# Kernel optimization log

Hardware: AMD Instinct MI355X
Metric: run time of the kernel (lower is better)

Reference implementation:

```python
import jax, jax.numpy as jnp
import numpy as np

B, S, D = 4, 2048, 1024
H, DK = 16, 64           # n_heads, d_kv; inner_dim = H*DK = 1024 = D
R = 16
SCALING = 32.0 / R       # lora_alpha / r = 2.0


def setup_inputs() -> dict:
    key = jax.random.key(0)
    ks = jax.random.split(key, 10)
    inner = H * DK
    sd = 1.0 / np.sqrt(D)
    return {
        "hidden_states": jax.random.normal(ks[0], (B, S, D), jnp.float32),
        "position_bias": jax.random.normal(ks[1], (1, H, S, S), jnp.float32),
        "Wq": jax.random.normal(ks[2], (inner, D), jnp.float32) * sd,
        "Wk": jax.random.normal(ks[3], (inner, D), jnp.float32) * sd,
        "Wv": jax.random.normal(ks[4], (inner, D), jnp.float32) * sd,
        "Wo": jax.random.normal(ks[5], (D, inner), jnp.float32) * sd,
        "Aq": jax.random.normal(ks[6], (R, D), jnp.float32) * sd,
        "Bq": jax.random.normal(ks[7], (inner, R), jnp.float32) * 0.01,
        "Av": jax.random.normal(ks[8], (R, D), jnp.float32) * sd,
        "Bv": jax.random.normal(ks[9], (inner, R), jnp.float32) * 0.01,
    }


def reference(hidden_states, position_bias, Wq, Wk, Wv, Wo, Aq, Bq, Av, Bv):
    x = hidden_states  # [B,S,D]

    def lora(w_a, w_b):
        # ((x @ A^T) @ B^T) * scaling; low-rank path, rank R
        return ((x @ w_a.T) @ w_b.T) * SCALING

    def heads(t):  # [B,S,H*DK] -> [B,H,S,DK]
        return t.reshape(B, S, H, DK).transpose(0, 2, 1, 3)

    q = heads(x @ Wq.T + lora(Aq, Bq))
    k = heads(x @ Wk.T)
    v = heads(x @ Wv.T + lora(Av, Bv))

    # T5-style: no 1/sqrt(d) scaling; additive position bias
    scores = jnp.einsum("bhqd,bhkd->bhqk", q, k) + position_bias
    attn = jax.nn.softmax(scores, axis=-1)
    out = jnp.einsum("bhqk,bhkd->bhqd", attn, v)
    out = out.transpose(0, 2, 1, 3).reshape(B, S, H * DK)
    return out @ Wo.T
```

## Files before the change

### kernel.cpp

```cpp
#include <hip/hip_runtime.h>
#include <hip/hip_bf16.h>

typedef __bf16 bf16x8 __attribute__((ext_vector_type(8)));
typedef float  f32x4  __attribute__((ext_vector_type(4)));
typedef unsigned short u16;
typedef unsigned long long u64;

#define L2E 1.44269504089f

__device__ __forceinline__ u16 f2b(float f) {
    __bf16 h = (__bf16)f;
    return __builtin_bit_cast(u16, h);
}

typedef const __attribute__((address_space(1))) void* gas1_t;
typedef __attribute__((address_space(3))) void* las3_t;

__device__ __forceinline__ void gl_lds16(const void* g, void* l) {
    __builtin_amdgcn_global_load_lds((gas1_t)g, (las3_t)l, 16, 0, 0);
}


__global__ void cvt_bf16(const float* __restrict__ in, u16* __restrict__ out, int n4) {
    int i = blockIdx.x * 256 + threadIdx.x;
    if (i < n4) {
        float4 v = ((const float4*)in)[i];
        u64 pk = (u64)f2b(v.x) | ((u64)f2b(v.y) << 16) | ((u64)f2b(v.z) << 32) | ((u64)f2b(v.w) << 48);
        ((u64*)out)[i] = pk;
    }
}

__global__ void prep_wqkv(const float* __restrict__ Wq, const float* __restrict__ Wk,
                          const float* __restrict__ Wv, const float* __restrict__ Aq,
                          const float* __restrict__ Bq, const float* __restrict__ Av,
                          const float* __restrict__ Bv, u16* __restrict__ out) {
    int idx = blockIdx.x * 256 + threadIdx.x;
    int n = idx >> 10, j = idx & 1023;
    float v;
    if (n < 1024) {
        v = Wq[n * 1024 + j];
        const float* Br = Bq + n * 16;
        float s = 0.f;
#pragma unroll
        for (int r = 0; r < 16; ++r) s += Br[r] * Aq[r * 1024 + j];
        v += 2.0f * s;
    } else if (n < 2048) {
        v = Wk[(n - 1024) * 1024 + j];
    } else {
        int nn = n - 2048;
        v = Wv[nn * 1024 + j];
        const float* Br = Bv + nn * 16;
        float s = 0.f;
#pragma unroll
        for (int r = 0; r < 16; ++r) s += Br[r] * Av[r * 1024 + j];
        v += 2.0f * s;
    }
    out[idx] = f2b(v);
}


template <int EPI>
__global__ __launch_bounds__(256, 2)
void gemm_bt(const u16* __restrict__ A, const u16* __restrict__ W,
             float* __restrict__ Cout,
             u16* __restrict__ qo, u16* __restrict__ ko, u16* __restrict__ vo,
             int M, int N, int K) {
    __shared__ u16 ldsA[128 * 32];
    __shared__ u16 ldsW[128 * 32];
    const int t = threadIdx.x;
    const int l = t & 63;
    const int m0 = blockIdx.y * 128;
    const int n0 = blockIdx.x * 128;
    const int wm = (t >> 6) >> 1, wn = (t >> 6) & 1;
    const int lc = l & 15, lg = l >> 4;

    const int srow = t >> 2;
    const int sby = ((t & 3) * 16) ^ ((srow & 3) << 4);
    const size_t Ar0 = (size_t)(m0 + srow) * K, Ar1 = (size_t)(m0 + srow + 64) * K;
    const size_t Wr0 = (size_t)(n0 + srow) * K, Wr1 = (size_t)(n0 + srow + 64) * K;
    char* dA = (char*)ldsA;
    char* dW = (char*)ldsW;
    const int d0 = srow * 64 + (t & 3) * 16;
    const int d1 = d0 + 4096;

    f32x4 acc[4][4];
#pragma unroll
    for (int i = 0; i < 4; ++i)
#pragma unroll
        for (int j = 0; j < 4; ++j) acc[i][j] = (f32x4)0.f;

    for (int kt = 0; kt < K; kt += 32) {
        const size_t kb = (size_t)kt * 2;
        gl_lds16((const char*)A + Ar0 * 2 + kb + sby, dA + d0);
        gl_lds16((const char*)A + Ar1 * 2 + kb + sby, dA + d1);
        gl_lds16((const char*)W + Wr0 * 2 + kb + sby, dW + d0);
        gl_lds16((const char*)W + Wr1 * 2 + kb + sby, dW + d1);
        __syncthreads();
        bf16x8 af[4], wf[4];
#pragma unroll
        for (int mi = 0; mi < 4; ++mi) {
            int row = wm * 64 + mi * 16 + lc;
            af[mi] = *(const bf16x8*)(dA + row * 64 + ((lg * 16) ^ ((row & 3) << 4)));
        }
#pragma unroll
        for (int ni = 0; ni < 4; ++ni) {
            int row = wn * 64 + ni * 16 + lc;
            wf[ni] = *(const bf16x8*)(dW + row * 64 + ((lg * 16) ^ ((row & 3) << 4)));
        }
#pragma unroll
        for (int mi = 0; mi < 4; ++mi)
#pragma unroll
            for (int ni = 0; ni < 4; ++ni)
                acc[mi][ni] = __builtin_amdgcn_mfma_f32_16x16x32_bf16(af[mi], wf[ni], acc[mi][ni], 0, 0, 0);
        __syncthreads();
    }

    if (EPI == 0) {
#pragma unroll
        for (int mi = 0; mi < 4; ++mi) {
            int row = m0 + wm * 64 + mi * 16 + lg * 4;
#pragma unroll
            for (int ni = 0; ni < 4; ++ni) {
                int col = n0 + wn * 64 + ni * 16 + lc;
#pragma unroll
                for (int r = 0; r < 4; ++r)
                    Cout[(size_t)(row + r) * N + col] = acc[mi][ni][r];
            }
        }
    } else {
#pragma unroll
        for (int mi = 0; mi < 4; ++mi) {
#pragma unroll
            for (int ni = 0; ni < 4; ++ni) {
                int n = n0 + wn * 64 + ni * 16 + lc;
                int which = n >> 10, inner = n & 1023;
                int h = inner >> 6, dk = inner & 63;
#pragma unroll
                for (int r = 0; r < 4; ++r) {
                    int mrow = m0 + wm * 64 + mi * 16 + lg * 4 + r;
                    int b = mrow >> 11, s = mrow & 2047;
                    size_t bh = (size_t)(b * 16 + h);
                    u16 v = f2b(acc[mi][ni][r]);
                    if (which == 0)      qo[(bh * 2048 + s) * 64 + dk] = v;
                    else if (which == 1) ko[(bh * 2048 + s) * 64 + dk] = v;
                    else                 vo[(bh * 64 + dk) * 2048 + s] = v;
                }
            }
        }
    }
}


__global__ __launch_bounds__(256, 2)
void attn(const u16* __restrict__ Qg, const u16* __restrict__ Kg,
          const u16* __restrict__ Vg, const float* __restrict__ bias,
          u16* __restrict__ Og) {
    __shared__ float biasb[2][32 * 66];
    __shared__ u16 pbuf[4][32 * 64];
    const int t = threadIdx.x;
    const int l = t & 63;
    const int w = t >> 6;
    const int h = blockIdx.x & 15;
    const int qt = blockIdx.x >> 4;
    const int q0 = qt * 32;
    const int lc = l & 15, lg = l >> 4;
    const size_t bh = (size_t)w * 16 + h;
    const u16* Qp = Qg + bh * 2048 * 64;
    const u16* Kp = Kg + bh * 2048 * 64;
    const u16* Vp = Vg + bh * 64 * 2048;
    char* pb = (char*)pbuf[w];

    const int srow = t >> 4;
    const int scol = (t & 15) * 4;
    const float* bst = bias + ((size_t)h * 2048 + q0 + srow) * 2048 + scol;
    float* bw0 = &biasb[0][srow * 66 + scol];
    float* bw1 = &biasb[1][srow * 66 + scol];

    bf16x8 qf[2][2];
#pragma unroll
    for (int mi = 0; mi < 2; ++mi)
#pragma unroll
        for (int ks = 0; ks < 2; ++ks)
            qf[mi][ks] = *(const bf16x8*)&Qp[(size_t)(q0 + mi * 16 + lc) * 64 + lg * 8 + ks * 32];

    f32x4 acc[2][4];
    float lsum[2][4];
#pragma unroll
    for (int mi = 0; mi < 2; ++mi) {
#pragma unroll
        for (int j = 0; j < 4; ++j) acc[mi][j] = (f32x4)0.f;
#pragma unroll
        for (int r = 0; r < 4; ++r) lsum[mi][r] = 0.f;
    }

    bf16x8 kf[2][4], vf[2][4];
#pragma unroll
    for (int ks = 0; ks < 2; ++ks)
#pragma unroll
        for (int ni = 0; ni < 4; ++ni) {
            kf[ks][ni] = *(const bf16x8*)&Kp[(size_t)(ni * 16 + lc) * 64 + lg * 8 + ks * 32];
            vf[ks][ni] = *(const bf16x8*)&Vp[(size_t)(ni * 16 + lc) * 2048 + lg * 8 + ks * 32];
        }
    {
        float4 a = *(const float4*)(bst);
        float4 b = *(const float4*)(bst + 16 * 2048);
        ((float2*)bw0)[0] = make_float2(a.x, a.y);
        ((float2*)bw0)[1] = make_float2(a.z, a.w);
        ((float2*)(bw0 + 16 * 66))[0] = make_float2(b.x, b.y);
        ((float2*)(bw0 + 16 * 66))[1] = make_float2(b.z, b.w);
    }
    float4 bra = *(const float4*)(bst + 64);
    float4 brb = *(const float4*)(bst + 16 * 2048 + 64);
    __syncthreads();

    for (int kt = 0; kt < 32; ++kt) {
        const int k0 = kt * 64;
        const int cur = kt & 1;

        f32x4 sfr[2][4];
#pragma unroll
        for (int mi = 0; mi < 2; ++mi)
#pragma unroll
            for (int ni = 0; ni < 4; ++ni) sfr[mi][ni] = (f32x4)0.f;
#pragma unroll
        for (int ks = 0; ks < 2; ++ks)
#pragma unroll
            for (int mi = 0; mi < 2; ++mi)
#pragma unroll
                for (int ni = 0; ni < 4; ++ni)
                    sfr[mi][ni] = __builtin_amdgcn_mfma_f32_16x16x32_bf16(qf[mi][ks], kf[ks][ni], sfr[mi][ni], 0, 0, 0);

        if (kt < 31) {
#pragma unroll
            for (int ks = 0; ks < 2; ++ks)
#pragma unroll
                for (int ni = 0; ni < 4; ++ni)
                    kf[ks][ni] = *(const bf16x8*)&Kp[(size_t)(k0 + 64 + ni * 16 + lc) * 64 + lg * 8 + ks * 32];
        }

        if (kt < 31) {
            float* bw = cur ? bw0 : bw1;
            ((float2*)bw)[0] = make_float2(bra.x, bra.y);
            ((float2*)bw)[1] = make_float2(bra.z, bra.w);
            ((float2*)(bw + 16 * 66))[0] = make_float2(brb.x, brb.y);
            ((float2*)(bw + 16 * 66))[1] = make_float2(brb.z, brb.w);
        }

#pragma unroll
        for (int mi = 0; mi < 2; ++mi) {
            const float* bb = &biasb[cur][(mi * 16 + lg * 4) * 66 + lc];
#pragma unroll
            for (int ni = 0; ni < 4; ++ni)
#pragma unroll
                for (int r = 0; r < 4; ++r) {
                    float p = __builtin_amdgcn_exp2f((sfr[mi][ni][r] + bb[r * 66 + ni * 16]) * L2E);
                    lsum[mi][r] += p;
                    int row = mi * 16 + lg * 4 + r;
                    int off = row * 128 + ((((ni * 16 + lc) * 2)) ^ ((row & 7) << 4));
                    *(u16*)(pb + off) = f2b(p);
                }
        }

        if (kt < 30) {
            bra = *(const float4*)(bst + k0 + 128);
            brb = *(const float4*)(bst + 16 * 2048 + k0 + 128);
        }

#pragma unroll
        for (int ks = 0; ks < 2; ++ks) {
            bf16x8 pf[2];
#pragma unroll
            for (int mi = 0; mi < 2; ++mi) {
                int row = mi * 16 + lc;
                pf[mi] = *(const bf16x8*)(pb + row * 128 + ((lg * 16 + ks * 64) ^ ((row & 7) << 4)));
            }
#pragma unroll
            for (int mi = 0; mi < 2; ++mi)
#pragma unroll
                for (int oni = 0; oni < 4; ++oni)
                    acc[mi][oni] = __builtin_amdgcn_mfma_f32_16x16x32_bf16(pf[mi], vf[ks][oni], acc[mi][oni], 0, 0, 0);
        }

        if (kt < 31) {
#pragma unroll
            for (int ks = 0; ks < 2; ++ks)
#pragma unroll
                for (int ni = 0; ni < 4; ++ni)
                    vf[ks][ni] = *(const bf16x8*)&Vp[(size_t)(ni * 16 + lc) * 2048 + k0 + 64 + lg * 8 + ks * 32];
        }

        __syncthreads();
    }

#pragma unroll
    for (int mi = 0; mi < 2; ++mi)
#pragma unroll
        for (int d = 1; d < 16; d <<= 1)
#pragma unroll
            for (int r = 0; r < 4; ++r) lsum[mi][r] += __shfl_xor(lsum[mi][r], d);

#pragma unroll
    for (int mi = 0; mi < 2; ++mi) {
#pragma unroll
        for (int r = 0; r < 4; ++r) {
            int s = q0 + mi * 16 + lg * 4 + r;
            float inv = 1.0f / lsum[mi][r];
            size_t base = ((size_t)w * 2048 + s) * 1024 + h * 64;
#pragma unroll
            for (int oni = 0; oni < 4; ++oni)
                Og[base + oni * 16 + lc] = f2b(acc[mi][oni][r] * inv);
        }
    }
}


extern "C" void kernel_launch(void* const* d_in, const int* in_sizes, int n_in,
                              void* d_out, int out_size, void* d_ws, size_t ws_size,
                              hipStream_t stream) {
    const float* x    = (const float*)d_in[0];
    const float* bias = (const float*)d_in[1];
    const float* Wq   = (const float*)d_in[2];
    const float* Wk   = (const float*)d_in[3];
    const float* Wv   = (const float*)d_in[4];
    const float* Wo   = (const float*)d_in[5];
    const float* Aq   = (const float*)d_in[6];
    const float* Bq   = (const float*)d_in[7];
    const float* Av   = (const float*)d_in[8];
    const float* Bv   = (const float*)d_in[9];
    float* out = (float*)d_out;

    char* ws = (char*)d_ws;
    u16* xb   = (u16*)(ws);
    u16* wqkv = (u16*)(ws + (16ull << 20));
    u16* wob  = (u16*)(ws + (22ull << 20));
    u16* qw   = (u16*)(ws + (24ull << 20));
    u16* kw   = (u16*)(ws + (40ull << 20));
    u16* vw   = (u16*)(ws + (56ull << 20));

    cvt_bf16<<<8192, 256, 0, stream>>>(x, xb, 2097152);
    cvt_bf16<<<1024, 256, 0, stream>>>(Wo, wob, 262144);
    prep_wqkv<<<12288, 256, 0, stream>>>(Wq, Wk, Wv, Aq, Bq, Av, Bv, wqkv);
    gemm_bt<1><<<dim3(24, 64), 256, 0, stream>>>(xb, wqkv, nullptr, qw, kw, vw, 8192, 3072, 1024);
    attn<<<1024, 256, 0, stream>>>(qw, kw, vw, bias, xb);
    gemm_bt<0><<<dim3(8, 64), 256, 0, stream>>>(xb, wob, out, nullptr, nullptr, nullptr, 8192, 1024, 1024);
}
```

Before: 402.6 us.

## Stage K/V tiles in LDS shared by four query-tile waves per batch-head

The attention kernel now gives each block four waves that work on different query tiles of the same batch-head, rather than four batches. K and V tiles are loaded once per block into double-buffered LDS with async global-to-LDS copies and then shared by all waves. The score MFMA is transposed (K as the A operand), so each lane holds one query column across keys. This lets bias be read directly from global as float4 into registers instead of staged through LDS, and lets P be written as packed 64-bit stores. The change cuts redundant K/V global traffic and per-element LDS writes, but adds LDS pressure and requires a new grid decomposition that depends on the launch code.

Result: faster. 338.9 us (-15.8%).

```diff
diff --git a/kernel.cpp b/kernel.cpp
--- a/kernel.cpp
+++ b/kernel.cpp
@@ -155,157 +155,145 @@
 void attn(const u16* __restrict__ Qg, const u16* __restrict__ Kg,
           const u16* __restrict__ Vg, const float* __restrict__ bias,
           u16* __restrict__ Og) {
-    __shared__ float biasb[2][32 * 66];
-    __shared__ u16 pbuf[4][32 * 64];
+    __shared__ u16 Kb[2][4096];
+    __shared__ u16 Vb[2][4096];
+    __shared__ u16 pbuf[4][2048];
     const int t = threadIdx.x;
     const int l = t & 63;
     const int w = t >> 6;
-    const int h = blockIdx.x & 15;
-    const int qt = blockIdx.x >> 4;
-    const int q0 = qt * 32;
+    const int bid = blockIdx.x;
+    const int h = bid & 15, b = (bid >> 4) & 3, qt = bid >> 6;
+    const int q0 = qt * 128 + w * 32;
     const int lc = l & 15, lg = l >> 4;
-    const size_t bh = (size_t)w * 16 + h;
+    const int rkey = (lc & 7) << 4;
+    const size_t bh = (size_t)b * 16 + h;
     const u16* Qp = Qg + bh * 2048 * 64;
-    const u16* Kp = Kg + bh * 2048 * 64;
-    const u16* Vp = Vg + bh * 64 * 2048;
+    const char* Kpb = (const char*)(Kg + bh * 2048 * 64);
+    const char* Vpb = (const char*)(Vg + bh * 64 * 2048);
     char* pb = (char*)pbuf[w];
 
-    const int srow = t >> 4;
-    const int scol = (t & 15) * 4;
-    const float* bst = bias + ((size_t)h * 2048 + q0 + srow) * 2048 + scol;
-    float* bw0 = &biasb[0][srow * 66 + scol];
-    float* bw1 = &biasb[1][srow * 66 + scol];
+    const int row0 = w * 8 + (l >> 3);
+    const int row1 = row0 + 32;
+    const int scol2 = ((l & 7) * 16) ^ (((l >> 3) & 7) << 4);
+    const int ldst = w * 1024 + l * 16;
 
     bf16x8 qf[2][2];
 #pragma unroll
     for (int mi = 0; mi < 2; ++mi)
 #pragma unroll
         for (int ks = 0; ks < 2; ++ks)
-            qf[mi][ks] = *(const bf16x8*)&Qp[(size_t)(q0 + mi * 16 + lc) * 64 + lg * 8 + ks * 32];
+            qf[mi][ks] = *(const bf16x8*)&Qp[(size_t)(q0 + mi * 16 + lc) * 64 + ks * 32 + lg * 8];
 
     f32x4 acc[2][4];
-    float lsum[2][4];
+    float lsum[2];
 #pragma unroll
     for (int mi = 0; mi < 2; ++mi) {
 #pragma unroll
         for (int j = 0; j < 4; ++j) acc[mi][j] = (f32x4)0.f;
-#pragma unroll
-        for (int r = 0; r < 4; ++r) lsum[mi][r] = 0.f;
-    }
-
-    bf16x8 kf[2][4], vf[2][4];
-#pragma unroll
-    for (int ks = 0; ks < 2; ++ks)
-#pragma unroll
-        for (int ni = 0; ni < 4; ++ni) {
-            kf[ks][ni] = *(const bf16x8*)&Kp[(size_t)(ni * 16 + lc) * 64 + lg * 8 + ks * 32];
-            vf[ks][ni] = *(const bf16x8*)&Vp[(size_t)(ni * 16 + lc) * 2048 + lg * 8 + ks * 32];
-        }
-    {
-        float4 a = *(const float4*)(bst);
-        float4 b = *(const float4*)(bst + 16 * 2048);
-        ((float2*)bw0)[0] = make_float2(a.x, a.y);
-        ((float2*)bw0)[1] = make_float2(a.z, a.w);
-        ((float2*)(bw0 + 16 * 66))[0] = make_float2(b.x, b.y);
-        ((float2*)(bw0 + 16 * 66))[1] = make_float2(b.z, b.w);
-    }
-    float4 bra = *(const float4*)(bst + 64);
-    float4 brb = *(const float4*)(bst + 16 * 2048 + 64);
+        lsum[mi] = 0.f;
+    }
+
+    const float* bp0 = bias + ((size_t)h * 2048 + q0 + lc) * 2048 + lg * 4;
+
+    gl_lds16(Kpb + (size_t)row0 * 128 + scol2, (char*)Kb[0] + ldst);
+    gl_lds16(Kpb + (size_t)row1 * 128 + scol2, (char*)Kb[0] + 4096 + ldst);
+    gl_lds16(Vpb + (size_t)row0 * 4096 + scol2, (char*)Vb[0] + ldst);
+    gl_lds16(Vpb + (size_t)row1 * 4096 + scol2, (char*)Vb[0] + 4096 + ldst);
+    float4 br[2][4];
+#pragma unroll
+    for (int mi = 0; mi < 2; ++mi)
+#pragma unroll
+        for (int ni = 0; ni < 4; ++ni)
+            br[mi][ni] = *(const float4*)(bp0 + (size_t)mi * 16 * 2048 + ni * 16);
     __syncthreads();
 
     for (int kt = 0; kt < 32; ++kt) {
+        const int cur = kt & 1;
         const int k0 = kt * 64;
-        const int cur = kt & 1;
-
-        f32x4 sfr[2][4];
-#pragma unroll
-        for (int mi = 0; mi < 2; ++mi)
-#pragma unroll
-            for (int ni = 0; ni < 4; ++ni) sfr[mi][ni] = (f32x4)0.f;
-#pragma unroll
-        for (int ks = 0; ks < 2; ++ks)
+
+        f32x4 sfr[4][2];
+#pragma unroll
+        for (int ni = 0; ni < 4; ++ni)
+#pragma unroll
+            for (int mi = 0; mi < 2; ++mi) sfr[ni][mi] = (f32x4)0.f;
+#pragma unroll
+        for (int ks = 0; ks < 2; ++ks) {
+            bf16x8 kf[4];
+#pragma unroll
+            for (int ni = 0; ni < 4; ++ni)
+                kf[ni] = *(const bf16x8*)((const char*)Kb[cur] + (ni * 16 + lc) * 128 + ((ks * 64 + lg * 16) ^ rkey));
+#pragma unroll
+            for (int ni = 0; ni < 4; ++ni)
+#pragma unroll
+                for (int mi = 0; mi < 2; ++mi)
+                    sfr[ni][mi] = __builtin_amdgcn_mfma_f32_16x16x32_bf16(kf[ni], qf[mi][ks], sfr[ni][mi], 0, 0, 0);
+        }
+
+        if (kt < 31) {
+            const size_t kb = (size_t)(k0 + 64);
+            gl_lds16(Kpb + (kb + row0) * 128 + scol2, (char*)Kb[cur ^ 1] + ldst);
+            gl_lds16(Kpb + (kb + row1) * 128 + scol2, (char*)Kb[cur ^ 1] + 4096 + ldst);
+            gl_lds16(Vpb + (size_t)row0 * 4096 + kb * 2 + scol2, (char*)Vb[cur ^ 1] + ldst);
+            gl_lds16(Vpb + (size_t)row1 * 4096 + kb * 2 + scol2, (char*)Vb[cur ^ 1] + 4096 + ldst);
+        }
+
+#pragma unroll
+        for (int mi = 0; mi < 2; ++mi) {
+            char* prb = pb + (mi * 16 + lc) * 128;
+#pragma unroll
+            for (int ni = 0; ni < 4; ++ni) {
+                u16 hh[4];
+#pragma unroll
+                for (int r = 0; r < 4; ++r) {
+                    float p = __builtin_amdgcn_exp2f((sfr[ni][mi][r] + (&br[mi][ni].x)[r]) * L2E);
+                    lsum[mi] += p;
+                    hh[r] = f2b(p);
+                }
+                u64 pk = (u64)hh[0] | ((u64)hh[1] << 16) | ((u64)hh[2] << 32) | ((u64)hh[3] << 48);
+                *(u64*)(prb + ((ni * 32 + lg * 8) ^ rkey)) = pk;
+            }
+        }
+
+        if (kt < 31) {
 #pragma unroll
             for (int mi = 0; mi < 2; ++mi)
 #pragma unroll
                 for (int ni = 0; ni < 4; ++ni)
-                    sfr[mi][ni] = __builtin_amdgcn_mfma_f32_16x16x32_bf16(qf[mi][ks], kf[ks][ni], sfr[mi][ni], 0, 0, 0);
-
-        if (kt < 31) {
-#pragma unroll
-            for (int ks = 0; ks < 2; ++ks)
-#pragma unroll
-                for (int ni = 0; ni < 4; ++ni)
-                    kf[ks][ni] = *(const bf16x8*)&Kp[(size_t)(k0 + 64 + ni * 16 + lc) * 64 + lg * 8 + ks * 32];
-        }
-
-        if (kt < 31) {
-            float* bw = cur ? bw0 : bw1;
-            ((float2*)bw)[0] = make_float2(bra.x, bra.y);
-            ((float2*)bw)[1] = make_float2(bra.z, bra.w);
-            ((float2*)(bw + 16 * 66))[0] = make_float2(brb.x, brb.y);
-            ((float2*)(bw + 16 * 66))[1] = make_float2(brb.z, brb.w);
-        }
-
-#pragma unroll
-        for (int mi = 0; mi < 2; ++mi) {
-            const float* bb = &biasb[cur][(mi * 16 + lg * 4) * 66 + lc];
-#pragma unroll
-            for (int ni = 0; ni < 4; ++ni)
-#pragma unroll
-                for (int r = 0; r < 4; ++r) {
-                    float p = __builtin_amdgcn_exp2f((sfr[mi][ni][r] + bb[r * 66 + ni * 16]) * L2E);
-                    lsum[mi][r] += p;
-                    int row = mi * 16 + lg * 4 + r;
-                    int off = row * 128 + ((((ni * 16 + lc) * 2)) ^ ((row & 7) << 4));
-                    *(u16*)(pb + off) = f2b(p);
-                }
-        }
-
-        if (kt < 30) {
-            bra = *(const float4*)(bst + k0 + 128);
-            brb = *(const float4*)(bst + 16 * 2048 + k0 + 128);
+                    br[mi][ni] = *(const float4*)(bp0 + (size_t)mi * 16 * 2048 + k0 + 64 + ni * 16);
         }
 
 #pragma unroll
         for (int ks = 0; ks < 2; ++ks) {
-            bf16x8 pf[2];
-#pragma unroll
-            for (int mi = 0; mi < 2; ++mi) {
-                int row = mi * 16 + lc;
-                pf[mi] = *(const bf16x8*)(pb + row * 128 + ((lg * 16 + ks * 64) ^ ((row & 7) << 4)));
-            }
+            bf16x8 pf[2], vf[4];
 #pragma unroll
             for (int mi = 0; mi < 2; ++mi)
+                pf[mi] = *(const bf16x8*)(pb + (mi * 16 + lc) * 128 + ((ks * 64 + lg * 16) ^ rkey));
+#pragma unroll
+            for (int oni = 0; oni < 4; ++oni)
+                vf[oni] = *(const bf16x8*)((const char*)Vb[cur] + (oni * 16 + lc) * 128 + ((ks * 64 + lg * 16) ^ rkey));
+#pragma unroll
+            for (int mi = 0; mi < 2; ++mi)
 #pragma unroll
                 for (int oni = 0; oni < 4; ++oni)
-                    acc[mi][oni] = __builtin_amdgcn_mfma_f32_16x16x32_bf16(pf[mi], vf[ks][oni], acc[mi][oni], 0, 0, 0);
-        }
-
-        if (kt < 31) {
-#pragma unroll
-            for (int ks = 0; ks < 2; ++ks)
-#pragma unroll
-                for (int ni = 0; ni < 4; ++ni)
-                    vf[ks][ni] = *(const bf16x8*)&Vp[(size_t)(ni * 16 + lc) * 2048 + k0 + 64 + lg * 8 + ks * 32];
+                    acc[mi][oni] = __builtin_amdgcn_mfma_f32_16x16x32_bf16(pf[mi], vf[oni], acc[mi][oni], 0, 0, 0);
         }
 
         __syncthreads();
     }
 
 #pragma unroll
-    for (int mi = 0; mi < 2; ++mi)
-#pragma unroll
-        for (int d = 1; d < 16; d <<= 1)
-#pragma unroll
-            for (int r = 0; r < 4; ++r) lsum[mi][r] += __shfl_xor(lsum[mi][r], d);
+    for (int mi = 0; mi < 2; ++mi) {
+        lsum[mi] += __shfl_xor(lsum[mi], 16);
+        lsum[mi] += __shfl_xor(lsum[mi], 32);
+    }
 
 #pragma unroll
     for (int mi = 0; mi < 2; ++mi) {
 #pragma unroll
         for (int r = 0; r < 4; ++r) {
             int s = q0 + mi * 16 + lg * 4 + r;
-            float inv = 1.0f / lsum[mi][r];
-            size_t base = ((size_t)w * 2048 + s) * 1024 + h * 64;
+            float inv = 1.0f / __shfl(lsum[mi], lg * 4 + r);
+            size_t base = ((size_t)b * 2048 + s) * 1024 + h * 64;
 #pragma unroll
             for (int oni = 0; oni < 4; ++oni)
                 Og[base + oni * 16 + lc] = f2b(acc[mi][oni][r] * inv);
```
